# Kernel optimization log

Measured on AMD Instinct MI355X. Metric: run time of the kernel, lower is better.

The kernel has to match this reference:

```python
import jax, jax.numpy as jnp
import numpy as np

N, F_IN, HID, E, G = 100000, 256, 256, 800000, 256


def setup_inputs() -> dict:
    key = jax.random.key(0)
    ks = jax.random.split(key, 10)
    x = jax.random.normal(ks[0], (N, F_IN), dtype=jnp.float32)
    edge_index = jax.random.randint(ks[1], (2, E), 0, N, dtype=jnp.int64)
    batch = jnp.sort(jax.random.randint(ks[2], (N,), 0, G, dtype=jnp.int64))
    s = 1.0 / np.sqrt(HID)
    W1 = jax.random.normal(ks[3], (F_IN, HID), dtype=jnp.float32) * s
    b1 = jnp.zeros((HID,), dtype=jnp.float32)
    W2 = jax.random.normal(ks[4], (HID, HID), dtype=jnp.float32) * s
    b2 = jnp.zeros((HID,), dtype=jnp.float32)
    Wc1 = jax.random.normal(ks[5], (HID, HID // 2), dtype=jnp.float32) * s
    bc1 = jnp.zeros((HID // 2,), dtype=jnp.float32)
    Wc2 = jax.random.normal(ks[6], (HID // 2, 2), dtype=jnp.float32) * s
    bc2 = jnp.zeros((2,), dtype=jnp.float32)
    return dict(x=x, edge_index=edge_index, batch=batch, num_graphs=G,
                W1=W1, b1=b1, W2=W2, b2=b2, Wc1=Wc1, bc1=bc1, Wc2=Wc2, bc2=bc2)


def _gcn_layer(h, src, dst, inv_sqrt_deg, W, b):
    # GCNConv: D^-1/2 (A + I) D^-1/2 (h W) + b
    hw = h @ W                                            # (N, H)
    coef = inv_sqrt_deg[src] * inv_sqrt_deg[dst]          # (E,)
    msgs = hw[src] * coef[:, None]                        # (E, H)
    agg = jax.ops.segment_sum(msgs, dst, num_segments=h.shape[0])
    self_loop = hw * (inv_sqrt_deg * inv_sqrt_deg)[:, None]
    return agg + self_loop + b


def reference(x, edge_index, batch, num_graphs, W1, b1, W2, b2, Wc1, bc1, Wc2, bc2):
    n = x.shape[0]
    src, dst = edge_index[0], edge_index[1]
    # degree with self-loops (symmetric normalization)
    deg = jax.ops.segment_sum(jnp.ones((src.shape[0],), jnp.float32), dst,
                              num_segments=n) + 1.0
    inv_sqrt_deg = jax.lax.rsqrt(deg)

    h = jax.nn.relu(_gcn_layer(x, src, dst, inv_sqrt_deg, W1, b1))
    node_emb = jax.nn.relu(_gcn_layer(h, src, dst, inv_sqrt_deg, W2, b2))

    # per-graph mean pooling (segment mean replacing the Python loop)
    sums = jax.ops.segment_sum(node_emb, batch, num_segments=num_graphs)
    counts = jax.ops.segment_sum(jnp.ones((n,), jnp.float32), batch,
                                 num_segments=num_graphs)
    graph_emb = sums / jnp.maximum(counts, 1.0)[:, None]

    # classifier MLP (dropout is identity in eval mode)
    hcls = jax.nn.relu(graph_emb @ Wc1 + bc1)
    logits = hcls @ Wc2 + bc2                             # (G, 2)
    return logits, node_emb
```

## Files before the change

### kernel.cpp

```cpp
#include <hip/hip_runtime.h>
#include <hip/hip_bf16.h>

#define HID 256
#define NGRAPH 256

typedef __bf16 bf16_t;
typedef __attribute__((ext_vector_type(8))) __bf16 bf16x8;
typedef __attribute__((ext_vector_type(4))) __bf16 bf16x4;
typedef __attribute__((ext_vector_type(4))) float f32x4;

__global__ __launch_bounds__(256) void prep_kernel(
    int* __restrict__ degi, int N, int ZB,
    const float* __restrict__ W1, bf16_t* __restrict__ Wf1,
    const float* __restrict__ W2, bf16_t* __restrict__ Wf2) {
    int b = blockIdx.x;
    if (b < ZB) {
        int i = b * 256 + threadIdx.x;
        if (i < N) degi[i] = 0;
        return;
    }
    int gi = (b - ZB) * 256 + threadIdx.x;
    const float* W = (gi < 65536) ? W1 : W2;
    bf16_t* Wf = (gi < 65536) ? Wf1 : Wf2;
    int idx = gi & 65535;
    float w = W[idx];
    int k = idx >> 8, n = idx & 255;
    int k0 = k >> 5, kg = (k >> 3) & 3, j = k & 7;
    int nt = n >> 4, m = n & 15;
    Wf[(size_t)(((k0 * 16 + nt) * 64) + kg * 16 + m) * 8 + j] = (bf16_t)w;
}

__global__ void count_bounds_kernel(const int* __restrict__ ei, int E, int CB,
                                    int* __restrict__ deg,
                                    const int* __restrict__ batch, int N, int G,
                                    int* __restrict__ gstart) {
    int b = blockIdx.x;
    if (b < CB) {
        int e = b * 256 + threadIdx.x;
        if (e < E) atomicAdd(&deg[ei[E + e]], 1);
        return;
    }
    int i = (b - CB) * 256 + threadIdx.x;
    if (i > N) return;
    int cur = (i < N) ? batch[i] : G;
    int prev = (i == 0) ? -1 : batch[i - 1];
    for (int g = prev + 1; g <= cur; ++g) gstart[g] = i;
}

#define SCHUNK 512

__global__ __launch_bounds__(256) void scan_pass1_kernel(
    const int* __restrict__ deg, int N, int* __restrict__ bsum) {
    __shared__ int red[256];
    int b = blockIdx.x, t = threadIdx.x;
    int i0 = b * SCHUNK + 2 * t;
    int v = 0;
    if (i0 < N) v += deg[i0];
    if (i0 + 1 < N) v += deg[i0 + 1];
    red[t] = v;
    __syncthreads();
    for (int s = 128; s > 0; s >>= 1) {
        if (t < s) red[t] += red[t + s];
        __syncthreads();
    }
    if (t == 0) bsum[b] = red[0];
}

__global__ __launch_bounds__(256) void scan_pass2_kernel(
    const int* __restrict__ bsum, int NB, int* __restrict__ boff) {
    __shared__ int s[256];
    int t = threadIdx.x;
    int v = (t < NB) ? bsum[t] : 0;
    s[t] = v;
    __syncthreads();
    for (int off = 1; off < 256; off <<= 1) {
        int x = s[t];
        if (t >= off) x += s[t - off];
        __syncthreads();
        s[t] = x;
        __syncthreads();
    }
    if (t < NB) boff[t] = s[t] - v;
}

__global__ __launch_bounds__(256) void scan_pass3_kernel(
    const int* __restrict__ deg, int N, const int* __restrict__ boff,
    int* __restrict__ rowptr, int* __restrict__ cursor, float* __restrict__ invd) {
    __shared__ int s[256];
    int b = blockIdx.x, t = threadIdx.x;
    int i0 = b * SCHUNK + 2 * t;
    int d0 = (i0 < N) ? deg[i0] : 0;
    int d1 = (i0 + 1 < N) ? deg[i0 + 1] : 0;
    int pair = d0 + d1;
    s[t] = pair;
    __syncthreads();
    for (int off = 1; off < 256; off <<= 1) {
        int x = s[t];
        if (t >= off) x += s[t - off];
        __syncthreads();
        s[t] = x;
        __syncthreads();
    }
    int excl = s[t] - pair + boff[b];
    if (i0 < N) {
        rowptr[i0] = excl;
        cursor[i0] = excl;
        invd[i0] = rsqrtf((float)d0 + 1.0f);
    }
    if (i0 + 1 < N) {
        int e1 = excl + d0;
        rowptr[i0 + 1] = e1;
        cursor[i0 + 1] = e1;
        invd[i0 + 1] = rsqrtf((float)d1 + 1.0f);
    }
}

__global__ void fill_csr_kernel(const int* __restrict__ ei, int E,
                                int* __restrict__ cursor, int* __restrict__ csr_src) {
    int e = blockIdx.x * blockDim.x + threadIdx.x;
    if (e >= E) return;
    int src = ei[e];
    int dst = ei[E + e];
    int pos = atomicAdd(&cursor[dst], 1);
    csr_src[pos] = src;
}

#define GBM 128

template <int INFP32>
__global__ __launch_bounds__(512, 4) void gemm_mfma_kernel(
    const void* __restrict__ Xv, const bf16_t* __restrict__ Wf,
    const float* __restrict__ rowscale, bf16_t* __restrict__ out, int Nrows) {
    __shared__ bf16_t Blds[32768];

    const int tid = threadIdx.x;
    const int wave = tid >> 6;
    const int lane = tid & 63;
    const int row0 = blockIdx.x * GBM;
    const int m = lane & 15;
    const int kg = lane >> 4;

    const int arow_raw = row0 + wave * 16 + m;
    const int arow = (arow_raw < Nrows) ? arow_raw : 0;

    f32x4 acc[16];
#pragma unroll
    for (int i = 0; i < 16; ++i) acc[i] = (f32x4){0.f, 0.f, 0.f, 0.f};

#pragma unroll
    for (int c = 0; c < 2; ++c) {
        float4 xa0, xb0, xa1, xb1, xa2, xb2, xa3, xb3;
        bf16x8 ah0, ah1, ah2, ah3;
        if (INFP32) {
            const float* xr = (const float*)Xv + (size_t)arow * 256 + c * 128 + kg * 8;
            xa0 = *(const float4*)&xr[0];   xb0 = *(const float4*)&xr[4];
            xa1 = *(const float4*)&xr[32];  xb1 = *(const float4*)&xr[36];
            xa2 = *(const float4*)&xr[64];  xb2 = *(const float4*)&xr[68];
            xa3 = *(const float4*)&xr[96];  xb3 = *(const float4*)&xr[100];
        } else {
            const bf16_t* xr = (const bf16_t*)Xv + (size_t)arow * 256 + c * 128 + kg * 8;
            ah0 = *(const bf16x8*)&xr[0];
            ah1 = *(const bf16x8*)&xr[32];
            ah2 = *(const bf16x8*)&xr[64];
            ah3 = *(const bf16x8*)&xr[96];
        }

        if (c) __syncthreads();
#pragma unroll
        for (int it = 0; it < 8; ++it)
            *(bf16x8*)&Blds[it * 4096 + tid * 8] =
                *(const bf16x8*)&Wf[c * 32768 + it * 4096 + tid * 8];
        __syncthreads();

#pragma unroll
        for (int k0c = 0; k0c < 4; ++k0c) {
            bf16x8 ah;
            if (INFP32) {
                float4 xa = (k0c == 0) ? xa0 : (k0c == 1) ? xa1 : (k0c == 2) ? xa2 : xa3;
                float4 xb = (k0c == 0) ? xb0 : (k0c == 1) ? xb1 : (k0c == 2) ? xb2 : xb3;
                float xf[8] = {xa.x, xa.y, xa.z, xa.w, xb.x, xb.y, xb.z, xb.w};
#pragma unroll
                for (int q = 0; q < 8; ++q) ah[q] = (bf16_t)xf[q];
            } else {
                ah = (k0c == 0) ? ah0 : (k0c == 1) ? ah1 : (k0c == 2) ? ah2 : ah3;
            }
#pragma unroll
            for (int nt = 0; nt < 16; ++nt) {
                bf16x8 bh = *(const bf16x8*)&Blds[(k0c * 16 + nt) * 512 + lane * 8];
                acc[nt] = __builtin_amdgcn_mfma_f32_16x16x32_bf16(ah, bh, acc[nt], 0, 0, 0);
            }
        }
    }

    const int rbase = row0 + wave * 16 + kg * 4;
#pragma unroll
    for (int j = 0; j < 4; ++j) {
        int r = rbase + j;
        if (r < Nrows) {
            float sc = rowscale[r];
#pragma unroll
            for (int nt = 0; nt < 16; ++nt)
                out[(size_t)r * 256 + nt * 16 + m] = (bf16_t)(acc[nt][j] * sc);
        }
    }
}

template <typename OutT>
__global__ __launch_bounds__(256) void gcn_aggregate_kernel(
    const bf16_t* __restrict__ hs, const int* __restrict__ rowptr,
    const int* __restrict__ deg, const int* __restrict__ csr_src,
    const float* __restrict__ inv_d, const float* __restrict__ bias,
    OutT* __restrict__ out, int N) {
    int gwid = (blockIdx.x * blockDim.x + threadIdx.x) >> 6;
    int lane = threadIdx.x & 63;
    int node = gwid * 2 + (lane >> 5);
    int hl = lane & 31;
    if (node >= N) return;
    int base = rowptr[node];
    int len = deg[node];
    int c = hl * 8;

    bf16x8 sv = *(const bf16x8*)&hs[(size_t)node * 256 + c];
    float a0[8], a1[8];
#pragma unroll
    for (int q = 0; q < 8; ++q) { a0[q] = (float)sv[q]; a1[q] = 0.f; }

    int i = 0;
    for (; i + 4 <= len; i += 4) {
        int s0 = csr_src[base + i];
        int s1 = csr_src[base + i + 1];
        int s2 = csr_src[base + i + 2];
        int s3 = csr_src[base + i + 3];
        bf16x8 v0 = *(const bf16x8*)&hs[(size_t)s0 * 256 + c];
        bf16x8 v1 = *(const bf16x8*)&hs[(size_t)s1 * 256 + c];
        bf16x8 v2 = *(const bf16x8*)&hs[(size_t)s2 * 256 + c];
        bf16x8 v3 = *(const bf16x8*)&hs[(size_t)s3 * 256 + c];
#pragma unroll
        for (int q = 0; q < 8; ++q) {
            a0[q] += (float)v0[q] + (float)v2[q];
            a1[q] += (float)v1[q] + (float)v3[q];
        }
    }
    for (; i < len; ++i) {
        int s = csr_src[base + i];
        bf16x8 v = *(const bf16x8*)&hs[(size_t)s * 256 + c];
#pragma unroll
        for (int q = 0; q < 8; ++q) a0[q] += (float)v[q];
    }

    float sc = inv_d[node];
    float4 bbA = *(const float4*)&bias[c];
    float4 bbB = *(const float4*)&bias[c + 4];
    float bb[8] = {bbA.x, bbA.y, bbA.z, bbA.w, bbB.x, bbB.y, bbB.z, bbB.w};
    float o[8];
#pragma unroll
    for (int q = 0; q < 8; ++q)
        o[q] = fmaxf(fmaf(a0[q] + a1[q], sc, bb[q]), 0.f);

    if constexpr (sizeof(OutT) == 2) {
        bf16x8 ov;
#pragma unroll
        for (int q = 0; q < 8; ++q) ov[q] = (bf16_t)o[q];
        *(bf16x8*)&out[(size_t)node * 256 + c] = ov;
    } else {
        float4 oA = {o[0], o[1], o[2], o[3]};
        float4 oB = {o[4], o[5], o[6], o[7]};
        *(float4*)&out[(size_t)node * 256 + c] = oA;
        *(float4*)&out[(size_t)node * 256 + c + 4] = oB;
    }
}

__global__ __launch_bounds__(256) void pool_mean_kernel(
    const float* __restrict__ emb, const int* __restrict__ gstart,
    float* __restrict__ gemb) {
    __shared__ float red[4][64];
    int g = blockIdx.x;
    int col = blockIdx.y * 64 + (threadIdx.x & 63);
    int rg = threadIdx.x >> 6;
    int s = gstart[g], e = gstart[g + 1];
    float sum = 0.f;
    for (int n = s + rg; n < e; n += 4) sum += emb[(size_t)n * 256 + col];
    red[rg][threadIdx.x & 63] = sum;
    __syncthreads();
    if (rg == 0) {
        int l = threadIdx.x & 63;
        float t = (red[0][l] + red[1][l]) + (red[2][l] + red[3][l]);
        float cnt = fmaxf((float)(e - s), 1.0f);
        gemb[g * 256 + col] = t / cnt;
    }
}

__global__ __launch_bounds__(128) void cls_kernel(
    const float* __restrict__ gemb, const float* __restrict__ Wc1,
    const float* __restrict__ bc1, const float* __restrict__ Wc2,
    const float* __restrict__ bc2, float* __restrict__ logits) {
    __shared__ float hl[128];
    int g = blockIdx.x, j = threadIdx.x;
    float sum = bc1[j];
    for (int k = 0; k < 256; ++k) sum = fmaf(gemb[g * 256 + k], Wc1[k * 128 + j], sum);
    hl[j] = fmaxf(sum, 0.f);
    __syncthreads();
    if (j < 2) {
        float s = bc2[j];
        for (int k = 0; k < 128; ++k) s = fmaf(hl[k], Wc2[k * 2 + j], s);
        logits[g * 2 + j] = s;
    }
}

extern "C" void kernel_launch(void* const* d_in, const int* in_sizes, int n_in,
                              void* d_out, int out_size, void* d_ws, size_t ws_size,
                              hipStream_t stream) {
    const float* x   = (const float*)d_in[0];
    const int*   ei  = (const int*)d_in[1];
    const int*   batch = (const int*)d_in[2];
    const float* W1  = (const float*)d_in[4];
    const float* b1  = (const float*)d_in[5];
    const float* W2  = (const float*)d_in[6];
    const float* b2  = (const float*)d_in[7];
    const float* Wc1 = (const float*)d_in[8];
    const float* bc1 = (const float*)d_in[9];
    const float* Wc2 = (const float*)d_in[10];
    const float* bc2 = (const float*)d_in[11];

    const int N = in_sizes[0] / HID;
    const int E = in_sizes[1] / 2;
    const int G = NGRAPH;

    float* logits   = (float*)d_out;
    float* node_out = (float*)d_out + (size_t)G * 2;

    char* wsb = (char*)d_ws;
    size_t off = 0;
    auto alloc = [&](size_t bytes) -> void* {
        void* p = wsb + off;
        off += (bytes + 255) & ~(size_t)255;
        return p;
    };
    bf16_t* hs     = (bf16_t*)alloc((size_t)N * HID * 2);
    bf16_t* hb     = (bf16_t*)alloc((size_t)N * HID * 2);
    int*    rowptr = (int*)alloc((size_t)N * 4);
    int*    cursor = (int*)alloc((size_t)N * 4);
    int*    degi   = (int*)alloc((size_t)N * 4);
    int*    csr    = (int*)alloc((size_t)E * 4);
    float*  invd   = (float*)alloc((size_t)N * 4);
    int*    gstart = (int*)alloc((size_t)(G + 1) * 4);
    float*  gemb   = (float*)alloc((size_t)G * HID * 4);
    int*    bsum   = (int*)alloc(256 * 4);
    int*    boff   = (int*)alloc(256 * 4);
    bf16_t* wf1    = (bf16_t*)alloc((size_t)HID * HID * 2);
    bf16_t* wf2    = (bf16_t*)alloc((size_t)HID * HID * 2);
    (void)ws_size; (void)n_in; (void)out_size;

    const int NB = (N + SCHUNK - 1) / SCHUNK;
    const int ZB = (N + 255) / 256;
    const int CB = (E + 255) / 256;
    const int BB = (N + 1 + 255) / 256;

    prep_kernel<<<ZB + 2 * HID * HID / 256, 256, 0, stream>>>(degi, N, ZB, W1, wf1, W2, wf2);
    count_bounds_kernel<<<CB + BB, 256, 0, stream>>>(ei, E, CB, degi, batch, N, G, gstart);
    scan_pass1_kernel<<<NB, 256, 0, stream>>>(degi, N, bsum);
    scan_pass2_kernel<<<1, 256, 0, stream>>>(bsum, NB, boff);
    scan_pass3_kernel<<<NB, 256, 0, stream>>>(degi, N, boff, rowptr, cursor, invd);
    fill_csr_kernel<<<(E + 255) / 256, 256, 0, stream>>>(ei, E, cursor, csr);

    const int GB = (N + GBM - 1) / GBM;
    const int AB = ((N + 1) / 2 * 64 + 255) / 256;

    gemm_mfma_kernel<1><<<GB, 512, 0, stream>>>(x, wf1, invd, hs, N);
    gcn_aggregate_kernel<bf16_t><<<AB, 256, 0, stream>>>(
        hs, rowptr, degi, csr, invd, b1, hb, N);

    gemm_mfma_kernel<0><<<GB, 512, 0, stream>>>(hb, wf2, invd, hs, N);
    gcn_aggregate_kernel<float><<<AB, 256, 0, stream>>>(
        hs, rowptr, degi, csr, invd, b2, node_out, N);

    pool_mean_kernel<<<dim3(G, 4), 256, 0, stream>>>(node_out, gstart, gemb);
    cls_kernel<<<G, 128, 0, stream>>>(gemb, Wc1, bc1, Wc2, bc2, logits);
}
```

Baseline: 365.3 us.

## Fuse CSR fill into first GEMM launch and load weights via global_load_lds

Folds the CSR-fill pass into the first GEMM kernel as extra leading blocks, so the edge scatter overlaps with the dense matmul and one launch is removed. Weight tiles are now staged into LDS with direct global-to-LDS loads when the builtin exists, bypassing registers. The fill blocks still reserve the GEMM's 64KB LDS allocation, which may limit how many of them are resident at once. The direct-load path depends on the per-wave LDS base plus lane offset matching the old layout.

```diff
diff --git a/kernel.cpp b/kernel.cpp
--- a/kernel.cpp
+++ b/kernel.cpp
@@ -115,28 +115,31 @@
     }
 }
 
-__global__ void fill_csr_kernel(const int* __restrict__ ei, int E,
-                                int* __restrict__ cursor, int* __restrict__ csr_src) {
-    int e = blockIdx.x * blockDim.x + threadIdx.x;
-    if (e >= E) return;
-    int src = ei[e];
-    int dst = ei[E + e];
-    int pos = atomicAdd(&cursor[dst], 1);
-    csr_src[pos] = src;
-}
-
 #define GBM 128
 
 template <int INFP32>
-__global__ __launch_bounds__(512, 4) void gemm_mfma_kernel(
+__global__ __launch_bounds__(512, 4) void gemm_fill_kernel(
     const void* __restrict__ Xv, const bf16_t* __restrict__ Wf,
-    const float* __restrict__ rowscale, bf16_t* __restrict__ out, int Nrows) {
+    const float* __restrict__ rowscale, bf16_t* __restrict__ out, int Nrows,
+    const int* __restrict__ ei, int E, int FB,
+    int* __restrict__ cursor, int* __restrict__ csr_src) {
     __shared__ bf16_t Blds[32768];
+
+    if (blockIdx.x < FB) {
+        int e = blockIdx.x * 512 + threadIdx.x;
+        if (e < E) {
+            int src = ei[e];
+            int dst = ei[E + e];
+            int pos = atomicAdd(&cursor[dst], 1);
+            csr_src[pos] = src;
+        }
+        return;
+    }
 
     const int tid = threadIdx.x;
     const int wave = tid >> 6;
     const int lane = tid & 63;
-    const int row0 = blockIdx.x * GBM;
+    const int row0 = (blockIdx.x - FB) * GBM;
     const int m = lane & 15;
     const int kg = lane >> 4;
 
@@ -166,10 +169,25 @@
         }
 
         if (c) __syncthreads();
+
+#if __has_builtin(__builtin_amdgcn_global_load_lds)
+        {
+            const bf16_t* gsrc = Wf + c * 32768;
+            const int wbase = (tid >> 6) * 512;
+#pragma unroll
+            for (int it = 0; it < 8; ++it) {
+                __builtin_amdgcn_global_load_lds(
+                    (const __attribute__((address_space(1))) void*)(gsrc + it * 4096 + tid * 8),
+                    (__attribute__((address_space(3))) void*)(Blds + it * 4096 + wbase),
+                    16, 0, 0);
+            }
+        }
+#else
 #pragma unroll
         for (int it = 0; it < 8; ++it)
             *(bf16x8*)&Blds[it * 4096 + tid * 8] =
                 *(const bf16x8*)&Wf[c * 32768 + it * 4096 + tid * 8];
+#endif
         __syncthreads();
 
 #pragma unroll
@@ -361,16 +379,18 @@
     scan_pass1_kernel<<<NB, 256, 0, stream>>>(degi, N, bsum);
     scan_pass2_kernel<<<1, 256, 0, stream>>>(bsum, NB, boff);
     scan_pass3_kernel<<<NB, 256, 0, stream>>>(degi, N, boff, rowptr, cursor, invd);
-    fill_csr_kernel<<<(E + 255) / 256, 256, 0, stream>>>(ei, E, cursor, csr);
 
     const int GB = (N + GBM - 1) / GBM;
+    const int FB = (E + 511) / 512;
     const int AB = ((N + 1) / 2 * 64 + 255) / 256;
 
-    gemm_mfma_kernel<1><<<GB, 512, 0, stream>>>(x, wf1, invd, hs, N);
+    gemm_fill_kernel<1><<<FB + GB, 512, 0, stream>>>(
+        x, wf1, invd, hs, N, ei, E, FB, cursor, csr);
     gcn_aggregate_kernel<bf16_t><<<AB, 256, 0, stream>>>(
         hs, rowptr, degi, csr, invd, b1, hb, N);
 
-    gemm_mfma_kernel<0><<<GB, 512, 0, stream>>>(hb, wf2, invd, hs, N);
+    gemm_fill_kernel<0><<<GB, 512, 0, stream>>>(
+        hb, wf2, invd, hs, N, nullptr, 0, 0, nullptr, nullptr);
     gcn_aggregate_kernel<float><<<AB, 256, 0, stream>>>(
         hs, rowptr, degi, csr, invd, b2, node_out, N);
 
```

Result: no change. 371.8 us (+1.8%).
